# Performance work log

Hardware: AMD Instinct MI355X
Metric: run time of the kernel (lower is better)

Reference implementation:

```python
import jax, jax.numpy as jnp
import numpy as np

S, B, IN, H = 256, 64, 512, 1024


def setup_inputs() -> dict:
    key = jax.random.key(0)
    ks = jax.random.split(key, 17)
    sx = 1.0 / np.sqrt(IN)
    sh = 1.0 / np.sqrt(H)
    d = {"x": jax.random.normal(ks[0], (S, B, IN), dtype=jnp.float32)}
    names_x = ["Wfx", "Wix", "Wox", "Wcx"]
    names_h = ["Wfh", "Wih", "Woh", "Wch"]
    bn_x = ["bfx", "bix", "box", "bcx"]
    bn_h = ["bfh", "bih", "boh", "bch"]
    i = 1
    for w, b in zip(names_x, bn_x):
        d[w] = jax.random.uniform(ks[i], (H, IN), jnp.float32, -sx, sx); i += 1
        d[b] = jax.random.uniform(ks[i], (H,), jnp.float32, -sx, sx); i += 1
    for w, b in zip(names_h, bn_h):
        d[w] = jax.random.uniform(ks[i], (H, H), jnp.float32, -sh, sh); i += 1
        d[b] = jax.random.uniform(ks[i], (H,), jnp.float32, -sh, sh); i += 1
    return d


def _lstm(x, Wfx, bfx, Wix, bix, Wox, box, Wcx, bcx, Wfh, bfh, Wih, bih, Woh, boh, Wch, bch):
    # Stack the 4 input-projection linears into one GEMM over all timesteps.
    Wx = jnp.stack([Wfx, Wix, Wox, Wcx])          # (4, H, IN)
    bx = jnp.stack([bfx, bix, box, bcx])          # (4, H)
    Wh = jnp.stack([Wfh, Wih, Woh, Wch])          # (4, H, H)
    bh = jnp.stack([bfh, bih, boh, bch])          # (4, H)
    gx = jnp.einsum('sbi,ghi->sbgh', x, Wx) + bx  # (S, B, 4, H)

    def step(carry, gx_t):
        h, c = carry
        gh = jnp.einsum('bk,ghk->bgh', h, Wh) + bh  # (B, 4, H)
        g = gx_t + gh
        f = jax.nn.sigmoid(g[:, 0])
        i = jax.nn.sigmoid(g[:, 1])
        o = jax.nn.sigmoid(g[:, 2])
        c_new = f * c + i * jnp.tanh(g[:, 3])
        h_new = o * jnp.tanh(c_new)
        return (h_new, c_new), h_new

    h0 = jnp.zeros((x.shape[1], Wfh.shape[0]), x.dtype)
    c0 = jnp.zeros_like(h0)
    (h_f, c_f), h_seq = jax.lax.scan(step, (h0, c0), gx)
    return h_seq, h_f[None], c_f[None]


def reference(x, Wfx, bfx, Wix, bix, Wox, box, Wcx, bcx, Wfh, bfh, Wih, bih, Woh, boh, Wch, bch):
    h_seq, h, c = _lstm(x, Wfx, bfx, Wix, bix, Wox, box, Wcx, bcx,
                        Wfh, bfh, Wih, bih, Woh, boh, Wch, bch)
    return h_seq, h, c
```

## Files before the change

kernel.cpp:

```cpp
#include <hip/hip_runtime.h>
#include <hip/hip_bf16.h>

typedef short short8 __attribute__((ext_vector_type(8)));
typedef float f32x4 __attribute__((ext_vector_type(4)));
typedef unsigned long long u64;
typedef unsigned u32;

constexpr int S = 256, B = 64, IN = 512, H = 1024;
constexpr int M = S * B;
constexpr int NG = 4 * H;

__global__ void f2b(const float* __restrict__ s, __hip_bfloat16* __restrict__ d, int n4) {
  int i = blockIdx.x * blockDim.x + threadIdx.x;
  if (i >= n4) return;
  float4 v = reinterpret_cast<const float4*>(s)[i];
  __hip_bfloat16 o[4] = {__float2bfloat16(v.x), __float2bfloat16(v.y),
                         __float2bfloat16(v.z), __float2bfloat16(v.w)};
  *reinterpret_cast<uint2*>(d + 4 * (size_t)i) = *reinterpret_cast<uint2*>(o);
}

__global__ void wconv(const float* w0, const float* w1, const float* w2, const float* w3,
                      const float* w4, const float* w5, const float* w6, const float* w7,
                      __hip_bfloat16* __restrict__ wxb, __hip_bfloat16* __restrict__ whb) {
  const int QX = H * IN / 4;
  const int QH = H * H / 4;
  int i = blockIdx.x * blockDim.x + threadIdx.x;
  const float* src;
  __hip_bfloat16* dst;
  int off;
  if (i < 4 * QX) {
    int g = i / QX; off = i - g * QX;
    src = g == 0 ? w0 : g == 1 ? w1 : g == 2 ? w2 : w3;
    dst = wxb + (size_t)g * H * IN;
  } else {
    int k = i - 4 * QX;
    if (k >= 4 * QH) return;
    int g = k / QH; off = k - g * QH;
    src = g == 0 ? w4 : g == 1 ? w5 : g == 2 ? w6 : w7;
    dst = whb + (size_t)g * H * H;
  }
  float4 v = reinterpret_cast<const float4*>(src)[off];
  __hip_bfloat16 o[4] = {__float2bfloat16(v.x), __float2bfloat16(v.y),
                         __float2bfloat16(v.z), __float2bfloat16(v.w)};
  *reinterpret_cast<uint2*>(dst + 4 * (size_t)off) = *reinterpret_cast<uint2*>(o);
}

__global__ void bias_k(const float* bx0, const float* bx1, const float* bx2, const float* bx3,
                       const float* bh0, const float* bh1, const float* bh2, const float* bh3,
                       float* bias) {
  int i = blockIdx.x * blockDim.x + threadIdx.x;
  if (i >= NG) return;
  int g = i >> 10, j = i & 1023;
  const float* bx = g == 0 ? bx0 : g == 1 ? bx1 : g == 2 ? bx2 : bx3;
  const float* bh = g == 0 ? bh0 : g == 1 ? bh1 : g == 2 ? bh2 : bh3;
  bias[i] = bx[j] + bh[j];
}

__global__ __launch_bounds__(256) void gx_gemm(const __hip_bfloat16* __restrict__ xb,
                                               const __hip_bfloat16* __restrict__ wxb,
                                               const float* __restrict__ bias,
                                               __hip_bfloat16* __restrict__ gx) {
  __shared__ __align__(16) ushort As[4][128][8];
  __shared__ __align__(16) ushort Bs[4][128][8];
  const int tid = threadIdx.x;
  const int l = tid & 63, w = tid >> 6;
  const int m0 = blockIdx.y * 128, n0 = blockIdx.x * 128;
  const int wm = (w >> 1) * 64, wn = (w & 1) * 64;
  const int cr = l & 15, kg = l >> 4;
  f32x4 acc[4][4] = {};

  ushort* Af = &As[0][0][0];
  ushort* Bfl = &Bs[0][0][0];

  for (int k0 = 0; k0 < IN; k0 += 32) {
    __syncthreads();
#pragma unroll
    for (int n = 0; n < 2; ++n) {
      int cA = w * 2 + n;
      int f = cA * 64 + l;
      const __hip_bfloat16* ga = xb + (size_t)(m0 + (f & 127)) * IN + k0 + (f >> 7) * 8;
      const __hip_bfloat16* gb = wxb + (size_t)(n0 + (f & 127)) * IN + k0 + (f >> 7) * 8;
      __builtin_amdgcn_global_load_lds((const u32*)ga, (u32*)(Af + cA * 512), 16, 0, 0);
      __builtin_amdgcn_global_load_lds((const u32*)gb, (u32*)(Bfl + cA * 512), 16, 0, 0);
    }
    __syncthreads();
    short8 a[4], b[4];
#pragma unroll
    for (int mi = 0; mi < 4; ++mi)
      a[mi] = *reinterpret_cast<const short8*>(&As[kg][wm + mi * 16 + cr][0]);
#pragma unroll
    for (int ni = 0; ni < 4; ++ni)
      b[ni] = *reinterpret_cast<const short8*>(&Bs[kg][wn + ni * 16 + cr][0]);
#pragma unroll
    for (int mi = 0; mi < 4; ++mi)
#pragma unroll
      for (int ni = 0; ni < 4; ++ni)
        acc[mi][ni] = __builtin_amdgcn_mfma_f32_16x16x32_bf16(a[mi], b[ni], acc[mi][ni], 0, 0, 0);
  }

#pragma unroll
  for (int ni = 0; ni < 4; ++ni) {
    int n = n0 + wn + ni * 16 + cr;
    float bv = bias[n];
    int g = n >> 10, j = n & 1023;
#pragma unroll
    for (int mi = 0; mi < 4; ++mi) {
#pragma unroll
      for (int r = 0; r < 4; ++r) {
        int m = m0 + wm + mi * 16 + kg * 4 + r;
        gx[((size_t)m * H + j) * 4 + g] = __float2bfloat16(acc[mi][ni][r] + bv);
      }
    }
  }
}

__device__ __forceinline__ u64 ldq(const u64* p) {
  return __hip_atomic_load(p, __ATOMIC_RELAXED, __HIP_MEMORY_SCOPE_AGENT);
}
__device__ __forceinline__ u32 ldw(const u32* p) {
  return __hip_atomic_load(p, __ATOMIC_RELAXED, __HIP_MEMORY_SCOPE_AGENT);
}
__device__ __forceinline__ void stw(u32* p, u32 v) {
  __hip_atomic_store(p, v, __ATOMIC_RELAXED, __HIP_MEMORY_SCOPE_AGENT);
}
__device__ __forceinline__ void stq(u64* p, u64 v) {
  __hip_atomic_store(p, v, __ATOMIC_RELAXED, __HIP_MEMORY_SCOPE_AGENT);
}
__device__ __forceinline__ float sigm(float x) {
  return __builtin_amdgcn_rcpf(1.f + __expf(-x));
}
__device__ __forceinline__ float tanhfast(float x) {
  return 2.f * __builtin_amdgcn_rcpf(1.f + __expf(-2.f * x)) - 1.f;
}
__device__ __forceinline__ void bar_lds() {
  asm volatile("s_waitcnt lgkmcnt(0)" ::: "memory");
  __builtin_amdgcn_sched_barrier(0);
  __builtin_amdgcn_s_barrier();
  __builtin_amdgcn_sched_barrier(0);
}

__global__ __launch_bounds__(256, 1) void lstm_rec(const __hip_bfloat16* __restrict__ whb,
                                                   const __hip_bfloat16* __restrict__ gx,
                                                   __hip_bfloat16* __restrict__ hx,
                                                   u32* __restrict__ flags,
                                                   float* __restrict__ out) {
  __shared__ __align__(16) ushort Bf[4][32][64][8];
  __shared__ __align__(16) float gt[4][4][16][20];
  const int tid = threadIdx.x;
  const int l = tid & 63, w = tid >> 6;
  const int jg = blockIdx.x & 63, bg = blockIdx.x >> 6;
  const int j0 = jg * 16, b0 = bg * 16;

  for (int idx = tid; idx < 4 * 32 * 64; idx += 256) {
    int g = idx >> 11, kb = (idx >> 6) & 31, ll = idx & 63;
    const __hip_bfloat16* src =
        whb + ((size_t)(g * H + j0 + (ll & 15))) * H + kb * 32 + (ll >> 4) * 8;
    *reinterpret_cast<uint4*>(&Bf[g][kb][ll][0]) = *reinterpret_cast<const uint4*>(src);
  }
  __syncthreads();

  const int cr = l & 15, kg = l >> 4;
  const int bi = tid >> 4, j = tid & 15;
  const u32* myfl = flags + (size_t)((bg << 6) + w * 16 + (l & 15)) * 16;
  u32* pubfl = flags + (size_t)((bg << 6) + jg) * 16;
  float c = 0.f;

  for (int t = 0; t < S; ++t) {
    const __hip_bfloat16* hsrc = hx + (size_t)(t & 1) * (B * H);
    __hip_bfloat16* hdst = hx + (size_t)((t + 1) & 1) * (B * H);

    const u64 gq = *reinterpret_cast<const u64*>(
        gx + ((size_t)(t * B + b0 + bi) * H + j0 + j) * 4);

    union { u64 q[2]; short8 s; } ua[8];
    if (t > 0) {
      while (!__all(ldw(myfl) >= (u32)t)) ;
      asm volatile("" ::: "memory");

      const u64* hp =
          reinterpret_cast<const u64*>(hsrc + (size_t)(b0 + cr) * H + w * 256 + kg * 8);
#pragma unroll
      for (int kk = 0; kk < 8; ++kk) {
        ua[kk].q[0] = ldq(hp + kk * 8);
        ua[kk].q[1] = ldq(hp + kk * 8 + 1);
      }
    } else {
#pragma unroll
      for (int kk = 0; kk < 8; ++kk) { ua[kk].q[0] = 0; ua[kk].q[1] = 0; }
    }

    f32x4 acc[4] = {};
#pragma unroll
    for (int kk = 0; kk < 8; ++kk) {
#pragma unroll
      for (int g = 0; g < 4; ++g) {
        short8 bv = *reinterpret_cast<const short8*>(&Bf[g][w * 8 + kk][l][0]);
        acc[g] = __builtin_amdgcn_mfma_f32_16x16x32_bf16(ua[kk].s, bv, acc[g], 0, 0, 0);
      }
    }
#pragma unroll
    for (int g = 0; g < 4; ++g)
      *reinterpret_cast<f32x4*>(&gt[w][g][cr][kg * 4]) = acc[g];
    bar_lds();

    float sf = 0.f, si = 0.f, so = 0.f, sc = 0.f;
#pragma unroll
    for (int wv = 0; wv < 4; ++wv) {
      sf += gt[wv][0][j][bi];
      si += gt[wv][1][j][bi];
      so += gt[wv][2][j][bi];
      sc += gt[wv][3][j][bi];
    }
    float gf = sf + __uint_as_float((u32)(gq & 0xffffu) << 16);
    float gi = si + __uint_as_float((u32)((gq >> 16) & 0xffffu) << 16);
    float go = so + __uint_as_float((u32)((gq >> 32) & 0xffffu) << 16);
    float gc = sc + __uint_as_float((u32)((gq >> 48) & 0xffffu) << 16);
    float f = sigm(gf);
    float i_ = sigm(gi);
    float o = sigm(go);
    float cn = f * c + i_ * tanhfast(gc);
    float hn = o * tanhfast(cn);
    c = cn;

    u32 hs16 = (u32)__bfloat16_as_ushort(__float2bfloat16(hn));
    u32 p1 = (hs16 & 0xffffu) | ((u32)__shfl_xor((int)hs16, 1) << 16);
    u32 p2 = (u32)__shfl_xor((int)p1, 2);
    if (t < S - 1) {
      if ((j & 3) == 0) {
        u64 pk = (u64)p1 | ((u64)p2 << 32);
        stq(reinterpret_cast<u64*>(hdst + (size_t)(b0 + bi) * H + j0 + j), pk);
      }
      asm volatile("s_waitcnt vmcnt(0)" ::: "memory");
      __builtin_amdgcn_sched_barrier(0);
      __builtin_amdgcn_s_barrier();
      __builtin_amdgcn_sched_barrier(0);
      if (tid == 0) stw(pubfl, (u32)(t + 1));
    }

    out[((size_t)(t * B + b0 + bi)) * H + j0 + j] = hn;
    if (t == S - 1) {
      out[(size_t)S * B * H + (size_t)(b0 + bi) * H + j0 + j] = hn;
      out[(size_t)S * B * H + (size_t)B * H + (size_t)(b0 + bi) * H + j0 + j] = cn;
    }
  }
}

extern "C" void kernel_launch(void* const* d_in, const int* in_sizes, int n_in,
                              void* d_out, int out_size, void* d_ws, size_t ws_size,
                              hipStream_t stream) {
  const float* x = (const float*)d_in[0];
  const float* Wx[4] = {(const float*)d_in[1], (const float*)d_in[3],
                        (const float*)d_in[5], (const float*)d_in[7]};
  const float* bx[4] = {(const float*)d_in[2], (const float*)d_in[4],
                        (const float*)d_in[6], (const float*)d_in[8]};
  const float* Wh[4] = {(const float*)d_in[9], (const float*)d_in[11],
                        (const float*)d_in[13], (const float*)d_in[15]};
  const float* bh[4] = {(const float*)d_in[10], (const float*)d_in[12],
                        (const float*)d_in[14], (const float*)d_in[16]};

  char* ws = (char*)d_ws;
  size_t o_flags = 0;
  size_t o_hx = 16384;
  size_t o_bias = o_hx + (size_t)2 * B * H * 2;
  size_t o_x = o_bias + (size_t)NG * 4;
  size_t o_wx = o_x + (size_t)M * IN * 2;
  size_t o_wh = o_wx + (size_t)NG * IN * 2;
  size_t o_gx = o_wh + (size_t)NG * H * 2;

  u32* flagsp = (u32*)(ws + o_flags);
  __hip_bfloat16* hxp = (__hip_bfloat16*)(ws + o_hx);
  float* biasp = (float*)(ws + o_bias);
  __hip_bfloat16* xb = (__hip_bfloat16*)(ws + o_x);
  __hip_bfloat16* wxb = (__hip_bfloat16*)(ws + o_wx);
  __hip_bfloat16* whb = (__hip_bfloat16*)(ws + o_wh);
  __hip_bfloat16* gxp = (__hip_bfloat16*)(ws + o_gx);

  hipMemsetAsync(ws, 0, 16384, stream);

  f2b<<<(M * IN / 4) / 256, 256, 0, stream>>>(x, xb, M * IN / 4);
  {
    int total4 = 4 * (H * IN / 4) + 4 * (H * H / 4);
    wconv<<<(total4 + 255) / 256, 256, 0, stream>>>(
        Wx[0], Wx[1], Wx[2], Wx[3], Wh[0], Wh[1], Wh[2], Wh[3], wxb, whb);
  }
  bias_k<<<NG / 256, 256, 0, stream>>>(bx[0], bx[1], bx[2], bx[3],
                                       bh[0], bh[1], bh[2], bh[3], biasp);

  dim3 gg(NG / 128, M / 128);
  gx_gemm<<<gg, 256, 0, stream>>>(xb, wxb, biasp, gxp);

  lstm_rec<<<256, 256, 0, stream>>>(whb, gxp, hxp, flagsp, (float*)d_out);
}
```

Measured before the change: 1.193 ms.

## Fuse input projection GEMM into recurrent LSTM kernel per timestep

Removes the separate gx GEMM and its bf16 intermediate buffer, and computes each gate's input projection inside the persistent recurrent kernel at every step. Each wave loads x and Wx slices from global memory and runs 16 extra MFMAs per step, adding the result to its gate accumulator, with the bias applied at the end. This avoids a large intermediate write/read and one launch, but lengthens the serial per-step critical path with extra loads and matrix ops.

```diff
diff --git a/kernel.cpp b/kernel.cpp
--- a/kernel.cpp
+++ b/kernel.cpp
@@ -56,64 +56,6 @@
   bias[i] = bx[j] + bh[j];
 }
 
-__global__ __launch_bounds__(256) void gx_gemm(const __hip_bfloat16* __restrict__ xb,
-                                               const __hip_bfloat16* __restrict__ wxb,
-                                               const float* __restrict__ bias,
-                                               __hip_bfloat16* __restrict__ gx) {
-  __shared__ __align__(16) ushort As[4][128][8];
-  __shared__ __align__(16) ushort Bs[4][128][8];
-  const int tid = threadIdx.x;
-  const int l = tid & 63, w = tid >> 6;
-  const int m0 = blockIdx.y * 128, n0 = blockIdx.x * 128;
-  const int wm = (w >> 1) * 64, wn = (w & 1) * 64;
-  const int cr = l & 15, kg = l >> 4;
-  f32x4 acc[4][4] = {};
-
-  ushort* Af = &As[0][0][0];
-  ushort* Bfl = &Bs[0][0][0];
-
-  for (int k0 = 0; k0 < IN; k0 += 32) {
-    __syncthreads();
-#pragma unroll
-    for (int n = 0; n < 2; ++n) {
-      int cA = w * 2 + n;
-      int f = cA * 64 + l;
-      const __hip_bfloat16* ga = xb + (size_t)(m0 + (f & 127)) * IN + k0 + (f >> 7) * 8;
-      const __hip_bfloat16* gb = wxb + (size_t)(n0 + (f & 127)) * IN + k0 + (f >> 7) * 8;
-      __builtin_amdgcn_global_load_lds((const u32*)ga, (u32*)(Af + cA * 512), 16, 0, 0);
-      __builtin_amdgcn_global_load_lds((const u32*)gb, (u32*)(Bfl + cA * 512), 16, 0, 0);
-    }
-    __syncthreads();
-    short8 a[4], b[4];
-#pragma unroll
-    for (int mi = 0; mi < 4; ++mi)
-      a[mi] = *reinterpret_cast<const short8*>(&As[kg][wm + mi * 16 + cr][0]);
-#pragma unroll
-    for (int ni = 0; ni < 4; ++ni)
-      b[ni] = *reinterpret_cast<const short8*>(&Bs[kg][wn + ni * 16 + cr][0]);
-#pragma unroll
-    for (int mi = 0; mi < 4; ++mi)
-#pragma unroll
-      for (int ni = 0; ni < 4; ++ni)
-        acc[mi][ni] = __builtin_amdgcn_mfma_f32_16x16x32_bf16(a[mi], b[ni], acc[mi][ni], 0, 0, 0);
-  }
-
-#pragma unroll
-  for (int ni = 0; ni < 4; ++ni) {
-    int n = n0 + wn + ni * 16 + cr;
-    float bv = bias[n];
-    int g = n >> 10, j = n & 1023;
-#pragma unroll
-    for (int mi = 0; mi < 4; ++mi) {
-#pragma unroll
-      for (int r = 0; r < 4; ++r) {
-        int m = m0 + wm + mi * 16 + kg * 4 + r;
-        gx[((size_t)m * H + j) * 4 + g] = __float2bfloat16(acc[mi][ni][r] + bv);
-      }
-    }
-  }
-}
-
 __device__ __forceinline__ u64 ldq(const u64* p) {
   return __hip_atomic_load(p, __ATOMIC_RELAXED, __HIP_MEMORY_SCOPE_AGENT);
 }
@@ -140,7 +82,9 @@
 }
 
 __global__ __launch_bounds__(256, 1) void lstm_rec(const __hip_bfloat16* __restrict__ whb,
-                                                   const __hip_bfloat16* __restrict__ gx,
+                                                   const __hip_bfloat16* __restrict__ xb,
+                                                   const __hip_bfloat16* __restrict__ wxb,
+                                                   const float* __restrict__ bias,
                                                    __hip_bfloat16* __restrict__ hx,
                                                    u32* __restrict__ flags,
                                                    float* __restrict__ out) {
@@ -163,14 +107,26 @@
   const int bi = tid >> 4, j = tid & 15;
   const u32* myfl = flags + (size_t)((bg << 6) + w * 16 + (l & 15)) * 16;
   u32* pubfl = flags + (size_t)((bg << 6) + jg) * 16;
+
+  float bias4[4];
+#pragma unroll
+  for (int g = 0; g < 4; ++g) bias4[g] = bias[(g << 10) + j0 + j];
+  const __hip_bfloat16* wxr = wxb + ((size_t)w * H + j0 + cr) * IN + kg * 8;
+
   float c = 0.f;
 
   for (int t = 0; t < S; ++t) {
     const __hip_bfloat16* hsrc = hx + (size_t)(t & 1) * (B * H);
     __hip_bfloat16* hdst = hx + (size_t)((t + 1) & 1) * (B * H);
 
-    const u64 gq = *reinterpret_cast<const u64*>(
-        gx + ((size_t)(t * B + b0 + bi) * H + j0 + j) * 4);
+    const __hip_bfloat16* xr = xb + ((size_t)(t * B) + b0 + cr) * IN + kg * 8;
+    short8 xa[16], wb[16];
+#pragma unroll
+    for (int kb = 0; kb < 16; ++kb) {
+      xa[kb] = *reinterpret_cast<const short8*>(xr + kb * 32);
+      wb[kb] = *reinterpret_cast<const short8*>(wxr + kb * 32);
+    }
+    asm volatile("" ::: "memory");
 
     union { u64 q[2]; short8 s; } ua[8];
     if (t > 0) {
@@ -189,6 +145,11 @@
       for (int kk = 0; kk < 8; ++kk) { ua[kk].q[0] = 0; ua[kk].q[1] = 0; }
     }
 
+    f32x4 gxacc = {};
+#pragma unroll
+    for (int kb = 0; kb < 16; ++kb)
+      gxacc = __builtin_amdgcn_mfma_f32_16x16x32_bf16(xa[kb], wb[kb], gxacc, 0, 0, 0);
+
     f32x4 acc[4] = {};
 #pragma unroll
     for (int kk = 0; kk < 8; ++kk) {
@@ -198,6 +159,7 @@
         acc[g] = __builtin_amdgcn_mfma_f32_16x16x32_bf16(ua[kk].s, bv, acc[g], 0, 0, 0);
       }
     }
+    acc[w] += gxacc;
 #pragma unroll
     for (int g = 0; g < 4; ++g)
       *reinterpret_cast<f32x4*>(&gt[w][g][cr][kg * 4]) = acc[g];
@@ -211,10 +173,10 @@
       so += gt[wv][2][j][bi];
       sc += gt[wv][3][j][bi];
     }
-    float gf = sf + __uint_as_float((u32)(gq & 0xffffu) << 16);
-    float gi = si + __uint_as_float((u32)((gq >> 16) & 0xffffu) << 16);
-    float go = so + __uint_as_float((u32)((gq >> 32) & 0xffffu) << 16);
-    float gc = sc + __uint_as_float((u32)((gq >> 48) & 0xffffu) << 16);
+    float gf = sf + bias4[0];
+    float gi = si + bias4[1];
+    float go = so + bias4[2];
+    float gc = sc + bias4[3];
     float f = sigm(gf);
     float i_ = sigm(gi);
     float o = sigm(go);
@@ -265,7 +227,6 @@
   size_t o_x = o_bias + (size_t)NG * 4;
   size_t o_wx = o_x + (size_t)M * IN * 2;
   size_t o_wh = o_wx + (size_t)NG * IN * 2;
-  size_t o_gx = o_wh + (size_t)NG * H * 2;
 
   u32* flagsp = (u32*)(ws + o_flags);
   __hip_bfloat16* hxp = (__hip_bfloat16*)(ws + o_hx);
@@ -273,7 +234,6 @@
   __hip_bfloat16* xb = (__hip_bfloat16*)(ws + o_x);
   __hip_bfloat16* wxb = (__hip_bfloat16*)(ws + o_wx);
   __hip_bfloat16* whb = (__hip_bfloat16*)(ws + o_wh);
-  __hip_bfloat16* gxp = (__hip_bfloat16*)(ws + o_gx);
 
   hipMemsetAsync(ws, 0, 16384, stream);
 
@@ -286,8 +246,5 @@
   bias_k<<<NG / 256, 256, 0, stream>>>(bx[0], bx[1], bx[2], bx[3],
                                        bh[0], bh[1], bh[2], bh[3], biasp);
 
-  dim3 gg(NG / 128, M / 128);
-  gx_gemm<<<gg, 256, 0, stream>>>(xb, wxb, biasp, gxp);
-
-  lstm_rec<<<256, 256, 0, stream>>>(whb, gxp, hxp, flagsp, (float*)d_out);
-}
+  lstm_rec<<<256, 256, 0, stream>>>(whb, xb, wxb, biasp, hxp, flagsp, (float*)d_out);
+}
```

New measurement: 1.447 ms. 21.2% more time.
